# Kernel tuning notes

Measured on AMD Instinct MI355X. Metric: run time of the kernel, lower is better.

## Reference

```python
import jax, jax.numpy as jnp
import numpy as np

N_REF = 4

def setup_inputs() -> dict:
    key = jax.random.key(0)
    ks = jax.random.split(key, 6)
    B, C, H, W = 4, 256, 64, 64
    s = 1.0 / np.sqrt(C)
    return {
        'x': jax.random.normal(ks[0], (B, C, H, W), jnp.float32),
        'Wq': jax.random.normal(ks[1], (C, C), jnp.float32) * s,
        'bq': jnp.zeros((C,), jnp.float32),
        'Wk': jax.random.normal(ks[2], (C, C), jnp.float32) * s,
        'bk': jnp.zeros((C,), jnp.float32),
        'Wv': jax.random.normal(ks[3], (C, C), jnp.float32) * s,
        'bv': jnp.zeros((C,), jnp.float32),
        'Woff': jax.random.normal(ks[4], (2 * N_REF, C), jnp.float32) * s,
        'boff': jnp.zeros((2 * N_REF,), jnp.float32),
    }

def _proj(x, W, b):
    # 1x1 conv == channel-mixing linear: [B,C,H,W] -> [B,O,H,W]
    return jnp.einsum('oc,bchw->bohw', W, x) + b[None, :, None, None]

def reference(x, Wq, bq, Wk, bk, Wv, bv, Woff, boff):
    B, C, H, W = x.shape
    n = N_REF
    HW = H * W
    Q = _proj(x, Wq, bq)
    K = _proj(x, Wk, bk)
    V = _proj(x, Wv, bv)
    offsets = _proj(Q, Woff, boff).reshape(B, n, 2, H, W)
    grid_h, grid_w = jnp.meshgrid(jnp.arange(H), jnp.arange(W), indexing='ij')
    ref_x = jnp.clip(jnp.round(grid_w[None, None] + offsets[:, :, 0]).astype(jnp.int32), 0, W - 1)
    ref_y = jnp.clip(jnp.round(grid_h[None, None] + offsets[:, :, 1]).astype(jnp.int32), 0, H - 1)
    ref_idx = (ref_y * W + ref_x).reshape(B, n, HW)          # [B,n,HW]
    K_flat = K.reshape(B, C, HW)
    V_flat = V.reshape(B, C, HW)
    # gather along spatial dim -> [B,C,n,HW]
    idx = ref_idx[:, None, :, :]                              # [B,1,n,HW]
    K_g = jnp.take_along_axis(K_flat[:, :, None, :], idx, axis=3)
    V_g = jnp.take_along_axis(V_flat[:, :, None, :], idx, axis=3)
    Q_flat = Q.reshape(B, C, HW)
    attn = jnp.einsum('bch,bcnh->bnh', Q_flat, K_g)
    attn = jax.nn.softmax(attn, axis=1)
    out = jnp.einsum('bnh,bcnh->bch', attn, V_g)
    return out.reshape(B, C, H, W)
```

## Files before the change

### kernel.cpp

```cpp
#include <hip/hip_runtime.h>
#include <math.h>

#define B_DIM   4
#define C_DIM   256
#define H_DIM   64
#define W_DIM   64
#define HW_DIM  4096
#define NPIX    (B_DIM * HW_DIM)
#define NREF    4
#define NJ      10

typedef unsigned short u16;
typedef __attribute__((ext_vector_type(4))) unsigned short u16x4;
typedef __attribute__((ext_vector_type(8))) unsigned short u16x8;
typedef __attribute__((ext_vector_type(8))) short bf16x8;
typedef __attribute__((ext_vector_type(4))) float f32x4;

__device__ __forceinline__ u16 bf16_rne(float f) {
    unsigned u = __float_as_uint(f);
    u = u + 0x7FFFu + ((u >> 16) & 1u);
    return (u16)(u >> 16);
}
__device__ __forceinline__ float bf16_tof(u16 h) {
    return __uint_as_float(((unsigned)h) << 16);
}
__device__ __forceinline__ void gload16(const void* g, void* l) {
    __builtin_amdgcn_global_load_lds(
        (const __attribute__((address_space(1))) void*)g,
        (__attribute__((address_space(3))) void*)l, 16, 0, 0);
}

__global__ __launch_bounds__(256) void prep1_kernel(
    const float* __restrict__ Wq, const float* __restrict__ bq,
    const float* __restrict__ Wk, const float* __restrict__ bk,
    const float* __restrict__ Woff, const float* __restrict__ boff,
    double* __restrict__ Weffp, double* __restrict__ beff,
    double* __restrict__ Mt)
{
    const int bx = blockIdx.x;
    const int t  = threadIdx.x;

    if (bx < 4 * NJ) {
        const int j  = bx >> 2;
        const int q  = bx & 3;
        const int o0 = q * 64;
        const float* Avec = (j < 8) ? (Woff + j * C_DIM) : ((j == 8) ? bq : bk);
        const float* Bmat = (j == 8) ? Wk : Wq;
        double s0 = 0, s1 = 0, s2 = 0, s3 = 0;
        for (int o = o0; o < o0 + 64; o += 4) {
            s0 += (double)Avec[o + 0] * (double)Bmat[(size_t)(o + 0) * C_DIM + t];
            s1 += (double)Avec[o + 1] * (double)Bmat[(size_t)(o + 1) * C_DIM + t];
            s2 += (double)Avec[o + 2] * (double)Bmat[(size_t)(o + 2) * C_DIM + t];
            s3 += (double)Avec[o + 3] * (double)Bmat[(size_t)(o + 3) * C_DIM + t];
        }
        Weffp[(size_t)(q * NJ + j) * C_DIM + t] = (s0 + s1) + (s2 + s3);

        if (q == 0 && j <= 8) {
            __shared__ double red[256];
            red[t] = (j < 8) ? (double)Woff[j * C_DIM + t] * (double)bq[t]
                             : (double)bq[t] * (double)bk[t];
            __syncthreads();
            for (int st = 128; st > 0; st >>= 1) {
                if (t < st) red[t] += red[t + st];
                __syncthreads();
            }
            if (t == 0) beff[j] = (j < 8) ? red[0] + (double)boff[j] : red[0];
        }
    } else {
        const int c = bx - 4 * NJ;
        __shared__ float wqcol[256];
        wqcol[t] = Wq[(size_t)t * C_DIM + c];
        __syncthreads();
        double a0 = 0, a1 = 0, a2 = 0, a3 = 0;
        for (int o = 0; o < C_DIM; o += 4) {
            a0 += (double)wqcol[o + 0] * (double)Wk[(size_t)(o + 0) * C_DIM + t];
            a1 += (double)wqcol[o + 1] * (double)Wk[(size_t)(o + 1) * C_DIM + t];
            a2 += (double)wqcol[o + 2] * (double)Wk[(size_t)(o + 2) * C_DIM + t];
            a3 += (double)wqcol[o + 3] * (double)Wk[(size_t)(o + 3) * C_DIM + t];
        }
        Mt[(size_t)c * C_DIM + t] = (a0 + a1) + (a2 + a3);
    }
}

__global__ __launch_bounds__(256) void prep2_kernel(
    const double* __restrict__ Mt, const float* __restrict__ Wv,
    u16* __restrict__ Bswh, u16* __restrict__ Bswl)
{
    const int T     = blockIdx.x;
    const int kt    = T & 3;
    const int ntile = (T >> 2) & 1;
    const int mat   = T >> 3;
    const int n0 = ntile * 128, k0 = kt * 64;
    const int t  = threadIdx.x;
    u16* dh = Bswh + (size_t)T * 8192;
    u16* dl = Bswl + (size_t)T * 8192;

#pragma unroll
    for (int it = 0; it < 4; ++it) {
        const int s   = it * 256 + t;
        const int row = s >> 3;
        const int ch  = s & 7;
        const int kk  = k0 + (ch ^ (row & 7)) * 8;
        float v[8];
        if (mat == 0) {
            const double* src = Mt + (size_t)(n0 + row) * C_DIM + kk;
#pragma unroll
            for (int i = 0; i < 8; ++i) v[i] = (float)src[i];
        } else {
            const float* src = Wv + (size_t)(n0 + row) * C_DIM + kk;
#pragma unroll
            for (int i = 0; i < 8; ++i) v[i] = src[i];
        }
        u16x8 hv, lv;
#pragma unroll
        for (int i = 0; i < 8; ++i) {
            hv[i] = bf16_rne(v[i]);
            lv[i] = bf16_rne(v[i] - bf16_tof(hv[i]));
        }
        *(u16x8*)(dh + (size_t)s * 8) = hv;
        if (mat == 0) *(u16x8*)(dl + (size_t)s * 8) = lv;
    }
}

__global__ __launch_bounds__(256) void xsplit_kernel(
    const float* __restrict__ x, const double* __restrict__ Weffp,
    u16* __restrict__ xh, u16* __restrict__ xl, double* __restrict__ part)
{
    __shared__ float  tile[64][65];
    __shared__ double wf[NJ][64];
    const int b   = blockIdx.z;
    const int cy  = blockIdx.y;
    const int c0  = cy * 64;
    const int hw0 = blockIdx.x * 64;
    const int t   = threadIdx.x;
    const int r4  = t >> 6;
    const int col = t & 63;

#pragma unroll
    for (int i = 0; i < 16; ++i) {
        const int row = i * 4 + r4;
        tile[row][col] = x[((size_t)b * C_DIM + c0 + row) * HW_DIM + hw0 + col];
    }
    for (int d = t; d < NJ * 64; d += 256) {
        const int jj = d >> 6, cc = d & 63;
        ((double*)wf)[d] = Weffp[(size_t)(0 * NJ + jj) * C_DIM + c0 + cc]
                         + Weffp[(size_t)(1 * NJ + jj) * C_DIM + c0 + cc]
                         + Weffp[(size_t)(2 * NJ + jj) * C_DIM + c0 + cc]
                         + Weffp[(size_t)(3 * NJ + jj) * C_DIM + c0 + cc];
    }
    __syncthreads();

#pragma unroll
    for (int i = 0; i < 16; ++i) {
        const int hwr = i * 4 + r4;
        const float v = tile[col][hwr];
        const u16 h = bf16_rne(v);
        const float lo = v - bf16_tof(h);
        const size_t o = ((size_t)b * HW_DIM + hw0 + hwr) * C_DIM + c0 + col;
        xh[o] = h;
        xl[o] = bf16_rne(lo);
    }

    const int p = col, g = r4;
    double a0 = 0, a1 = 0, a2 = 0;
    for (int c = 0; c < 64; ++c) {
        const double xv = (double)tile[c][p];
        a0 += wf[2 * g][c] * xv;
        a1 += wf[2 * g + 1][c] * xv;
        if (g < 2) a2 += wf[8 + g][c] * xv;
    }
    const int pix = b * HW_DIM + hw0 + p;
    part[(size_t)(cy * NJ + 2 * g) * NPIX + pix]     = a0;
    part[(size_t)(cy * NJ + 2 * g + 1) * NPIX + pix] = a1;
    if (g < 2) part[(size_t)(cy * NJ + 8 + g) * NPIX + pix] = a2;
}

__global__ __launch_bounds__(256) void idx_kernel(
    const double* __restrict__ part, const double* __restrict__ beff,
    int* __restrict__ idx_buf, float* __restrict__ kqf, float* __restrict__ vqf)
{
    const int pix = blockIdx.x * 256 + threadIdx.x;
    const int hw  = pix & (HW_DIM - 1);
    const int h   = hw >> 6;
    const int w   = hw & 63;

    double o[8];
#pragma unroll
    for (int j = 0; j < 8; ++j)
        o[j] = part[(size_t)(0 * NJ + j) * NPIX + pix] + part[(size_t)(1 * NJ + j) * NPIX + pix]
             + part[(size_t)(2 * NJ + j) * NPIX + pix] + part[(size_t)(3 * NJ + j) * NPIX + pix]
             + beff[j];

    int r[NREF];
#pragma unroll
    for (int n = 0; n < NREF; ++n) {
        const float ox = (float)o[2 * n];
        const float oy = (float)o[2 * n + 1];
        int rx = (int)rintf((float)w + ox);
        int ry = (int)rintf((float)h + oy);
        rx = min(max(rx, 0), W_DIM - 1);
        ry = min(max(ry, 0), H_DIM - 1);
        r[n] = ry * W_DIM + rx;
    }
    int4 outv; outv.x = r[0]; outv.y = r[1]; outv.z = r[2]; outv.w = r[3];
    *(int4*)(idx_buf + (size_t)pix * 4) = outv;

    const double kq = part[(size_t)(0 * NJ + 8) * NPIX + pix] + part[(size_t)(1 * NJ + 8) * NPIX + pix]
                    + part[(size_t)(2 * NJ + 8) * NPIX + pix] + part[(size_t)(3 * NJ + 8) * NPIX + pix];
    const double vq = part[(size_t)(0 * NJ + 9) * NPIX + pix] + part[(size_t)(1 * NJ + 9) * NPIX + pix]
                    + part[(size_t)(2 * NJ + 9) * NPIX + pix] + part[(size_t)(3 * NJ + 9) * NPIX + pix]
                    + beff[8];
    kqf[pix] = (float)kq;
    vqf[pix] = (float)vq;
}

__global__ __launch_bounds__(256) void qkv_mfma(
    const u16* __restrict__ xh, const u16* __restrict__ xl,
    const u16* __restrict__ Bswh, const u16* __restrict__ Bswl,
    const float* __restrict__ bv,
    float* __restrict__ Kpt, float* __restrict__ Vt)
{
    const int mat   = blockIdx.z;
    const int ntile = blockIdx.y;
    const int m0    = blockIdx.x * 64;
    const int n0    = ntile * 128;
    const bool three = (mat == 0);
    float* Out = mat ? Vt : Kpt;

    __shared__ u16 lds[24576];
    u16* Ah = lds;
    u16* Al = lds + 4096;
    u16* Bh = lds + 8192;
    u16* Bl = lds + 16384;

    const int t    = threadIdx.x;
    const int lane = t & 63;
    const int wv   = t >> 6;
    const int wm   = (wv >> 1) * 32;
    const int wn   = (wv & 1) * 64;

    f32x4 acc[2][4] = {};

    for (int kt = 0; kt < 4; ++kt) {
        const int k0 = kt * 64;
        const size_t Tb = (size_t)((mat * 2 + ntile) * 4 + kt) * 8192;

#pragma unroll
        for (int it = 0; it < 2; ++it) {
            const int s   = it * 256 + t;
            const int row = s >> 3;
            const int sch = (s & 7) ^ (row & 7);
            const size_t goff = (size_t)(m0 + row) * C_DIM + k0 + sch * 8;
            gload16(xh + goff, (char*)Ah + s * 16);
            if (three) gload16(xl + goff, (char*)Al + s * 16);
        }
#pragma unroll
        for (int it = 0; it < 4; ++it) {
            const int s = it * 256 + t;
            gload16(Bswh + Tb + (size_t)s * 8, (char*)Bh + s * 16);
            if (three) gload16(Bswl + Tb + (size_t)s * 8, (char*)Bl + s * 16);
        }
        __syncthreads();

#pragma unroll
        for (int ks = 0; ks < 2; ++ks) {
            bf16x8 afh[2], afl[2], bfh[4], bfl[4];
#pragma unroll
            for (int mt = 0; mt < 2; ++mt) {
                const int row = wm + mt * 16 + (lane & 15);
                const int ch  = (ks * 4 + (lane >> 4)) ^ (row & 7);
                const int off = row * 128 + ch * 16;
                afh[mt] = *(const bf16x8*)((const char*)Ah + off);
                if (three) afl[mt] = *(const bf16x8*)((const char*)Al + off);
            }
#pragma unroll
            for (int nt = 0; nt < 4; ++nt) {
                const int row = wn + nt * 16 + (lane & 15);
                const int ch  = (ks * 4 + (lane >> 4)) ^ (row & 7);
                const int off = row * 128 + ch * 16;
                bfh[nt] = *(const bf16x8*)((const char*)Bh + off);
                if (three) bfl[nt] = *(const bf16x8*)((const char*)Bl + off);
            }
#pragma unroll
            for (int mt = 0; mt < 2; ++mt)
#pragma unroll
                for (int nt = 0; nt < 4; ++nt) {
                    acc[mt][nt] = __builtin_amdgcn_mfma_f32_16x16x32_bf16(afh[mt], bfh[nt], acc[mt][nt], 0, 0, 0);
                    if (three) {
                        acc[mt][nt] = __builtin_amdgcn_mfma_f32_16x16x32_bf16(afh[mt], bfl[nt], acc[mt][nt], 0, 0, 0);
                        acc[mt][nt] = __builtin_amdgcn_mfma_f32_16x16x32_bf16(afl[mt], bfh[nt], acc[mt][nt], 0, 0, 0);
                    }
                }
        }
        __syncthreads();
    }

    const int col = lane & 15;
    const int rg  = (lane >> 4) * 4;
#pragma unroll
    for (int nt = 0; nt < 4; ++nt) {
        const int n = n0 + wn + nt * 16 + col;
        const float bias = mat ? bv[n] : 0.0f;
#pragma unroll
        for (int mt = 0; mt < 2; ++mt) {
            const int m = m0 + wm + mt * 16 + rg;
#pragma unroll
            for (int r = 0; r < 4; ++r)
                Out[(size_t)(m + r) * C_DIM + n] = acc[mt][nt][r] + bias;
        }
    }
}

__global__ __launch_bounds__(1024) void attn_kernel(
    const u16*   __restrict__ xh,
    const u16*   __restrict__ xl,
    const float* __restrict__ Kpt,
    const float* __restrict__ Vt,
    const int*   __restrict__ idx_buf,
    const float* __restrict__ kqf,
    const float* __restrict__ vqf,
    float* __restrict__ out)
{
    __shared__ float trans[16][260];

    const int t    = threadIdx.x;
    const int wave = t >> 6;
    const int lane = t & 63;

    const int pix0 = blockIdx.x * 16;
    const int b    = pix0 / HW_DIM;
    const int hw   = (pix0 % HW_DIM) + wave;
    const int pix  = b * HW_DIM + hw;

    const u16x4 hv = *(const u16x4*)(xh + (size_t)pix * C_DIM + lane * 4);
    const u16x4 lv = *(const u16x4*)(xl + (size_t)pix * C_DIM + lane * 4);
    float q[4];
#pragma unroll
    for (int i = 0; i < 4; ++i) q[i] = bf16_tof(hv[i]) + bf16_tof(lv[i]);

    const int4 iv = *(const int4*)(idx_buf + (size_t)pix * 4);
    int idx[NREF] = {iv.x, iv.y, iv.z, iv.w};
    const float vq = vqf[pix];

    float logit[NREF];
#pragma unroll
    for (int n = 0; n < NREF; ++n) {
        const float* krow = Kpt + ((size_t)b * HW_DIM + idx[n]) * C_DIM;
        float4 kv = *(const float4*)(krow + lane * 4);
        float lp = fmaf(q[3], kv.w, fmaf(q[2], kv.z, fmaf(q[1], kv.y, q[0] * kv.x)));
#pragma unroll
        for (int off = 1; off < 64; off <<= 1) lp += __shfl_xor(lp, off);
        logit[n] = lp + kqf[(size_t)b * HW_DIM + idx[n]] + vq;
    }

    float mx = fmaxf(fmaxf(logit[0], logit[1]), fmaxf(logit[2], logit[3]));
    float e[NREF], s = 0.0f;
#pragma unroll
    for (int n = 0; n < NREF; ++n) { e[n] = expf(logit[n] - mx); s += e[n]; }
    float wgt[NREF];
#pragma unroll
    for (int n = 0; n < NREF; ++n) wgt[n] = e[n] / s;

    float o4[4] = {0.f, 0.f, 0.f, 0.f};
#pragma unroll
    for (int n = 0; n < NREF; ++n) {
        const float* vrow = Vt + ((size_t)b * HW_DIM + idx[n]) * C_DIM;
        float4 vv = *(const float4*)(vrow + lane * 4);
        o4[0] = fmaf(wgt[n], vv.x, o4[0]);
        o4[1] = fmaf(wgt[n], vv.y, o4[1]);
        o4[2] = fmaf(wgt[n], vv.z, o4[2]);
        o4[3] = fmaf(wgt[n], vv.w, o4[3]);
    }

    *(float4*)&trans[wave][lane * 4] = *(float4*)o4;
    __syncthreads();

    float* ob = out + (size_t)b * C_DIM * HW_DIM + (pix0 % HW_DIM);
    const int px = t & 15;
#pragma unroll
    for (int cc = 0; cc < C_DIM; cc += 64) {
        const int c = cc + (t >> 4);
        ob[(size_t)c * HW_DIM + px] = trans[px][c];
    }
}

extern "C" void kernel_launch(void* const* d_in, const int* in_sizes, int n_in,
                              void* d_out, int out_size, void* d_ws, size_t ws_size,
                              hipStream_t stream) {
    const float* x    = (const float*)d_in[0];
    const float* Wq   = (const float*)d_in[1];
    const float* bq   = (const float*)d_in[2];
    const float* Wk   = (const float*)d_in[3];
    const float* bk   = (const float*)d_in[4];
    const float* Wv   = (const float*)d_in[5];
    const float* bv   = (const float*)d_in[6];
    const float* Woff = (const float*)d_in[7];
    const float* boff = (const float*)d_in[8];
    float* out = (float*)d_out;

    char* ws = (char*)d_ws;
    float*  Kpt   = (float*)ws;
    float*  Vt    = (float*)(ws + (size_t)16 * 1024 * 1024);
    u16*    xh    = (u16*)  (ws + (size_t)48 * 1024 * 1024);
    u16*    xl    = (u16*)  (ws + (size_t)56 * 1024 * 1024);
    char*   aux   = ws + (size_t)64 * 1024 * 1024;
    double* Weffp = (double*)(aux);
    double* beff  = (double*)(aux + 128 * 1024);
    int*    idxb  = (int*)   (aux + 192 * 1024);
    float*  kqf   = (float*) (aux + 448 * 1024);
    float*  vqf   = (float*) (aux + 512 * 1024);
    u16*    Bswh  = (u16*)   (aux + 576 * 1024);
    u16*    Bswl  = (u16*)   (aux + 832 * 1024);
    double* Mt    = (double*)(aux + 1088 * 1024);
    double* part  = (double*)(aux + 2 * 1024 * 1024);

    prep1_kernel<<<dim3(4 * NJ + 256), dim3(256), 0, stream>>>(
        Wq, bq, Wk, bk, Woff, boff, Weffp, beff, Mt);
    prep2_kernel<<<dim3(16), dim3(256), 0, stream>>>(Mt, Wv, Bswh, Bswl);
    xsplit_kernel<<<dim3(HW_DIM / 64, C_DIM / 64, B_DIM), dim3(256), 0, stream>>>(
        x, Weffp, xh, xl, part);
    idx_kernel<<<dim3(NPIX / 256), dim3(256), 0, stream>>>(part, beff, idxb, kqf, vqf);
    qkv_mfma<<<dim3(NPIX / 64, 2, 2), dim3(256), 0, stream>>>(
        xh, xl, Bswh, Bswl, bv, Kpt, Vt);
    attn_kernel<<<dim3(NPIX / 16), dim3(1024), 0, stream>>>(
        xh, xl, Kpt, Vt, idxb, kqf, vqf, out);
}
```

Measured before the change: 69.71 us.

## Merge prep kernels, widen QKV GEMM tile to full N, store V in bf16

The two weight-prep kernels become one launch. Wq^T·Wk is now computed directly in fp32 with an LDS-tiled GEMM and written out in swizzled hi/lo bf16 form, which removes the double-precision Mt intermediate. The QKV MFMA kernel now covers all 256 output columns per block, so the A tile is loaded once instead of twice, at the cost of more LDS and accumulators per block. V is stored as bf16 to halve gather traffic in the attention kernel, which loses some precision in V. The M matrix is now accumulated in fp32 rather than fp64.

```diff
diff --git a/kernel.cpp b/kernel.cpp
--- a/kernel.cpp
+++ b/kernel.cpp
@@ -30,12 +30,13 @@
         (__attribute__((address_space(3))) void*)l, 16, 0, 0);
 }
 
-__global__ __launch_bounds__(256) void prep1_kernel(
+__global__ __launch_bounds__(256) void prep_kernel(
     const float* __restrict__ Wq, const float* __restrict__ bq,
     const float* __restrict__ Wk, const float* __restrict__ bk,
+    const float* __restrict__ Wv,
     const float* __restrict__ Woff, const float* __restrict__ boff,
     double* __restrict__ Weffp, double* __restrict__ beff,
-    double* __restrict__ Mt)
+    u16* __restrict__ Bswh, u16* __restrict__ Bswl)
 {
     const int bx = blockIdx.x;
     const int t  = threadIdx.x;
@@ -66,59 +67,92 @@
             }
             if (t == 0) beff[j] = (j < 8) ? red[0] + (double)boff[j] : red[0];
         }
+    } else if (bx < 72) {
+        __shared__ float wq_s[64][32];
+        __shared__ float wk_s[64][64];
+        const int sub   = bx - 40;
+        const int T     = sub >> 2;
+        const int nsub  = sub & 3;
+        const int ntile = T >> 2;
+        const int kt    = T & 3;
+        const int nb    = ntile * 128 + nsub * 32;
+        const int kb    = kt * 64;
+
+        const int tx = t & 15;
+        const int ty = t >> 4;
+
+        float acc[2][4] = {};
+
+        for (int oc = 0; oc < 4; ++oc) {
+            const int o0 = oc * 64;
+#pragma unroll
+            for (int i = 0; i < 2; ++i) {
+                const int s = i * 256 + t;
+                const int row = s >> 3, c4 = (s & 7) * 4;
+                *(float4*)&wq_s[row][c4] =
+                    *(const float4*)(Wq + (size_t)(o0 + row) * C_DIM + nb + c4);
+            }
+#pragma unroll
+            for (int i = 0; i < 4; ++i) {
+                const int s = i * 256 + t;
+                const int row = s >> 4, c4 = (s & 15) * 4;
+                *(float4*)&wk_s[row][c4] =
+                    *(const float4*)(Wk + (size_t)(o0 + row) * C_DIM + kb + c4);
+            }
+            __syncthreads();
+#pragma unroll 4
+            for (int oo = 0; oo < 64; ++oo) {
+                const float2 a = *(const float2*)&wq_s[oo][ty * 2];
+                const float4 b4 = *(const float4*)&wk_s[oo][tx * 4];
+                acc[0][0] = fmaf(a.x, b4.x, acc[0][0]);
+                acc[0][1] = fmaf(a.x, b4.y, acc[0][1]);
+                acc[0][2] = fmaf(a.x, b4.z, acc[0][2]);
+                acc[0][3] = fmaf(a.x, b4.w, acc[0][3]);
+                acc[1][0] = fmaf(a.y, b4.x, acc[1][0]);
+                acc[1][1] = fmaf(a.y, b4.y, acc[1][1]);
+                acc[1][2] = fmaf(a.y, b4.z, acc[1][2]);
+                acc[1][3] = fmaf(a.y, b4.w, acc[1][3]);
+            }
+            __syncthreads();
+        }
+
+        u16* dh = Bswh + (size_t)T * 8192;
+        u16* dl = Bswl + (size_t)T * 8192;
+#pragma unroll
+        for (int j = 0; j < 2; ++j) {
+            const int rimg = nsub * 32 + ty * 2 + j;
+            const int base = rimg * 64 + (((tx >> 1) ^ (rimg & 7)) * 8) + (tx & 1) * 4;
+            u16x4 hv, lv;
+#pragma unroll
+            for (int i = 0; i < 4; ++i) {
+                hv[i] = bf16_rne(acc[j][i]);
+                lv[i] = bf16_rne(acc[j][i] - bf16_tof(hv[i]));
+            }
+            *(u16x4*)(dh + base) = hv;
+            *(u16x4*)(dl + base) = lv;
+        }
     } else {
-        const int c = bx - 4 * NJ;
-        __shared__ float wqcol[256];
-        wqcol[t] = Wq[(size_t)t * C_DIM + c];
-        __syncthreads();
-        double a0 = 0, a1 = 0, a2 = 0, a3 = 0;
-        for (int o = 0; o < C_DIM; o += 4) {
-            a0 += (double)wqcol[o + 0] * (double)Wk[(size_t)(o + 0) * C_DIM + t];
-            a1 += (double)wqcol[o + 1] * (double)Wk[(size_t)(o + 1) * C_DIM + t];
-            a2 += (double)wqcol[o + 2] * (double)Wk[(size_t)(o + 2) * C_DIM + t];
-            a3 += (double)wqcol[o + 3] * (double)Wk[(size_t)(o + 3) * C_DIM + t];
-        }
-        Mt[(size_t)c * C_DIM + t] = (a0 + a1) + (a2 + a3);
-    }
-}
-
-__global__ __launch_bounds__(256) void prep2_kernel(
-    const double* __restrict__ Mt, const float* __restrict__ Wv,
-    u16* __restrict__ Bswh, u16* __restrict__ Bswl)
-{
-    const int T     = blockIdx.x;
-    const int kt    = T & 3;
-    const int ntile = (T >> 2) & 1;
-    const int mat   = T >> 3;
-    const int n0 = ntile * 128, k0 = kt * 64;
-    const int t  = threadIdx.x;
-    u16* dh = Bswh + (size_t)T * 8192;
-    u16* dl = Bswl + (size_t)T * 8192;
-
-#pragma unroll
-    for (int it = 0; it < 4; ++it) {
-        const int s   = it * 256 + t;
-        const int row = s >> 3;
-        const int ch  = s & 7;
-        const int kk  = k0 + (ch ^ (row & 7)) * 8;
-        float v[8];
-        if (mat == 0) {
-            const double* src = Mt + (size_t)(n0 + row) * C_DIM + kk;
-#pragma unroll
-            for (int i = 0; i < 8; ++i) v[i] = (float)src[i];
-        } else {
-            const float* src = Wv + (size_t)(n0 + row) * C_DIM + kk;
-#pragma unroll
-            for (int i = 0; i < 8; ++i) v[i] = src[i];
-        }
-        u16x8 hv, lv;
-#pragma unroll
-        for (int i = 0; i < 8; ++i) {
-            hv[i] = bf16_rne(v[i]);
-            lv[i] = bf16_rne(v[i] - bf16_tof(hv[i]));
-        }
-        *(u16x8*)(dh + (size_t)s * 8) = hv;
-        if (mat == 0) *(u16x8*)(dl + (size_t)s * 8) = lv;
+        const int ti    = bx - 72;
+        const int kt    = ti & 3;
+        const int ntile = (ti >> 2) & 1;
+        const int Timg  = 8 + ti;
+        const int n0 = ntile * 128, k0 = kt * 64;
+        u16* dh = Bswh + (size_t)Timg * 8192;
+#pragma unroll
+        for (int it = 0; it < 4; ++it) {
+            const int s   = it * 256 + t;
+            const int row = s >> 3;
+            const int ch  = s & 7;
+            const int kk  = k0 + (ch ^ (row & 7)) * 8;
+            const float4 w0 = *(const float4*)(Wv + (size_t)(n0 + row) * C_DIM + kk);
+            const float4 w1 = *(const float4*)(Wv + (size_t)(n0 + row) * C_DIM + kk + 4);
+            u16x8 hv;
+            hv[0] = bf16_rne(w0.x); hv[1] = bf16_rne(w0.y);
+            hv[2] = bf16_rne(w0.z); hv[3] = bf16_rne(w0.w);
+            hv[4] = bf16_rne(w1.x); hv[5] = bf16_rne(w1.y);
+            hv[6] = bf16_rne(w1.z); hv[7] = bf16_rne(w1.w);
+            *(u16x8*)(dh + (size_t)s * 8) = hv;
+        }
     }
 }
 
@@ -218,32 +252,28 @@
     const u16* __restrict__ xh, const u16* __restrict__ xl,
     const u16* __restrict__ Bswh, const u16* __restrict__ Bswl,
     const float* __restrict__ bv,
-    float* __restrict__ Kpt, float* __restrict__ Vt)
+    float* __restrict__ Kpt, u16* __restrict__ Vtb)
 {
-    const int mat   = blockIdx.z;
-    const int ntile = blockIdx.y;
-    const int m0    = blockIdx.x * 64;
-    const int n0    = ntile * 128;
+    const int mat = blockIdx.x & 1;
+    const int m0  = (blockIdx.x >> 1) * 64;
     const bool three = (mat == 0);
-    float* Out = mat ? Vt : Kpt;
-
-    __shared__ u16 lds[24576];
+
+    __shared__ u16 lds[40960];
     u16* Ah = lds;
     u16* Al = lds + 4096;
     u16* Bh = lds + 8192;
-    u16* Bl = lds + 16384;
+    u16* Bl = lds + 24576;
 
     const int t    = threadIdx.x;
     const int lane = t & 63;
     const int wv   = t >> 6;
     const int wm   = (wv >> 1) * 32;
-    const int wn   = (wv & 1) * 64;
-
-    f32x4 acc[2][4] = {};
+    const int wn   = (wv & 1) * 128;
+
+    f32x4 acc[2][8] = {};
 
     for (int kt = 0; kt < 4; ++kt) {
         const int k0 = kt * 64;
-        const size_t Tb = (size_t)((mat * 2 + ntile) * 4 + kt) * 8192;
 
 #pragma unroll
         for (int it = 0; it < 2; ++it) {
@@ -255,16 +285,19 @@
             if (three) gload16(xl + goff, (char*)Al + s * 16);
         }
 #pragma unroll
-        for (int it = 0; it < 4; ++it) {
-            const int s = it * 256 + t;
-            gload16(Bswh + Tb + (size_t)s * 8, (char*)Bh + s * 16);
-            if (three) gload16(Bswl + Tb + (size_t)s * 8, (char*)Bl + s * 16);
+        for (int it = 0; it < 8; ++it) {
+            const int s  = it * 256 + t;
+            const int ni = s >> 10;
+            const int sl = s & 1023;
+            const size_t Tb = (size_t)((mat * 2 + ni) * 4 + kt) * 8192;
+            gload16(Bswh + Tb + (size_t)sl * 8, (char*)Bh + s * 16);
+            if (three) gload16(Bswl + Tb + (size_t)sl * 8, (char*)Bl + s * 16);
         }
         __syncthreads();
 
 #pragma unroll
         for (int ks = 0; ks < 2; ++ks) {
-            bf16x8 afh[2], afl[2], bfh[4], bfl[4];
+            bf16x8 afh[2], afl[2];
 #pragma unroll
             for (int mt = 0; mt < 2; ++mt) {
                 const int row = wm + mt * 16 + (lane & 15);
@@ -274,23 +307,29 @@
                 if (three) afl[mt] = *(const bf16x8*)((const char*)Al + off);
             }
 #pragma unroll
-            for (int nt = 0; nt < 4; ++nt) {
-                const int row = wn + nt * 16 + (lane & 15);
-                const int ch  = (ks * 4 + (lane >> 4)) ^ (row & 7);
-                const int off = row * 128 + ch * 16;
-                bfh[nt] = *(const bf16x8*)((const char*)Bh + off);
-                if (three) bfl[nt] = *(const bf16x8*)((const char*)Bl + off);
-            }
-#pragma unroll
-            for (int mt = 0; mt < 2; ++mt)
+            for (int ng = 0; ng < 2; ++ng) {
+                bf16x8 bfh[4], bfl[4];
 #pragma unroll
                 for (int nt = 0; nt < 4; ++nt) {
-                    acc[mt][nt] = __builtin_amdgcn_mfma_f32_16x16x32_bf16(afh[mt], bfh[nt], acc[mt][nt], 0, 0, 0);
-                    if (three) {
-                        acc[mt][nt] = __builtin_amdgcn_mfma_f32_16x16x32_bf16(afh[mt], bfl[nt], acc[mt][nt], 0, 0, 0);
-                        acc[mt][nt] = __builtin_amdgcn_mfma_f32_16x16x32_bf16(afl[mt], bfh[nt], acc[mt][nt], 0, 0, 0);
+                    const int row = wn + ng * 64 + nt * 16 + (lane & 15);
+                    const int ch  = (ks * 4 + (lane >> 4)) ^ (row & 7);
+                    const int off = row * 128 + ch * 16;
+                    bfh[nt] = *(const bf16x8*)((const char*)Bh + off);
+                    if (three) bfl[nt] = *(const bf16x8*)((const char*)Bl + off);
+                }
+#pragma unroll
+                for (int mt = 0; mt < 2; ++mt)
+#pragma unroll
+                    for (int nt = 0; nt < 4; ++nt) {
+                        f32x4 a = acc[mt][ng * 4 + nt];
+                        a = __builtin_amdgcn_mfma_f32_16x16x32_bf16(afh[mt], bfh[nt], a, 0, 0, 0);
+                        if (three) {
+                            a = __builtin_amdgcn_mfma_f32_16x16x32_bf16(afh[mt], bfl[nt], a, 0, 0, 0);
+                            a = __builtin_amdgcn_mfma_f32_16x16x32_bf16(afl[mt], bfh[nt], a, 0, 0, 0);
+                        }
+                        acc[mt][ng * 4 + nt] = a;
                     }
-                }
+            }
         }
         __syncthreads();
     }
@@ -298,24 +337,29 @@
     const int col = lane & 15;
     const int rg  = (lane >> 4) * 4;
 #pragma unroll
-    for (int nt = 0; nt < 4; ++nt) {
-        const int n = n0 + wn + nt * 16 + col;
-        const float bias = mat ? bv[n] : 0.0f;
-#pragma unroll
-        for (int mt = 0; mt < 2; ++mt) {
-            const int m = m0 + wm + mt * 16 + rg;
-#pragma unroll
-            for (int r = 0; r < 4; ++r)
-                Out[(size_t)(m + r) * C_DIM + n] = acc[mt][nt][r] + bias;
-        }
-    }
+    for (int ng = 0; ng < 2; ++ng)
+#pragma unroll
+        for (int nt = 0; nt < 4; ++nt) {
+            const int n = wn + ng * 64 + nt * 16 + col;
+            const float bias = mat ? bv[n] : 0.0f;
+#pragma unroll
+            for (int mt = 0; mt < 2; ++mt) {
+                const int m = m0 + wm + mt * 16 + rg;
+#pragma unroll
+                for (int r = 0; r < 4; ++r) {
+                    const float v = acc[mt][ng * 4 + nt][r] + bias;
+                    if (mat) Vtb[(size_t)(m + r) * C_DIM + n] = bf16_rne(v);
+                    else     Kpt[(size_t)(m + r) * C_DIM + n] = v;
+                }
+            }
+        }
 }
 
 __global__ __launch_bounds__(1024) void attn_kernel(
     const u16*   __restrict__ xh,
     const u16*   __restrict__ xl,
     const float* __restrict__ Kpt,
-    const float* __restrict__ Vt,
+    const u16*   __restrict__ Vtb,
     const int*   __restrict__ idx_buf,
     const float* __restrict__ kqf,
     const float* __restrict__ vqf,
@@ -364,12 +408,11 @@
     float o4[4] = {0.f, 0.f, 0.f, 0.f};
 #pragma unroll
     for (int n = 0; n < NREF; ++n) {
-        const float* vrow = Vt + ((size_t)b * HW_DIM + idx[n]) * C_DIM;
-        float4 vv = *(const float4*)(vrow + lane * 4);
-        o4[0] = fmaf(wgt[n], vv.x, o4[0]);
-        o4[1] = fmaf(wgt[n], vv.y, o4[1]);
-        o4[2] = fmaf(wgt[n], vv.z, o4[2]);
-        o4[3] = fmaf(wgt[n], vv.w, o4[3]);
+        const u16x4 vv = *(const u16x4*)(Vtb + ((size_t)b * HW_DIM + idx[n]) * C_DIM + lane * 4);
+        o4[0] = fmaf(wgt[n], bf16_tof(vv[0]), o4[0]);
+        o4[1] = fmaf(wgt[n], bf16_tof(vv[1]), o4[1]);
+        o4[2] = fmaf(wgt[n], bf16_tof(vv[2]), o4[2]);
+        o4[3] = fmaf(wgt[n], bf16_tof(vv[3]), o4[3]);
     }
 
     *(float4*)&trans[wave][lane * 4] = *(float4*)o4;
@@ -400,7 +443,7 @@
 
     char* ws = (char*)d_ws;
     float*  Kpt   = (float*)ws;
-    float*  Vt    = (float*)(ws + (size_t)16 * 1024 * 1024);
+    u16*    Vtb   = (u16*)  (ws + (size_t)16 * 1024 * 1024);
     u16*    xh    = (u16*)  (ws + (size_t)48 * 1024 * 1024);
     u16*    xl    = (u16*)  (ws + (size_t)56 * 1024 * 1024);
     char*   aux   = ws + (size_t)64 * 1024 * 1024;
@@ -411,17 +454,15 @@
     float*  vqf   = (float*) (aux + 512 * 1024);
     u16*    Bswh  = (u16*)   (aux + 576 * 1024);
     u16*    Bswl  = (u16*)   (aux + 832 * 1024);
-    double* Mt    = (double*)(aux + 1088 * 1024);
     double* part  = (double*)(aux + 2 * 1024 * 1024);
 
-    prep1_kernel<<<dim3(4 * NJ + 256), dim3(256), 0, stream>>>(
-        Wq, bq, Wk, bk, Woff, boff, Weffp, beff, Mt);
-    prep2_kernel<<<dim3(16), dim3(256), 0, stream>>>(Mt, Wv, Bswh, Bswl);
+    prep_kernel<<<dim3(80), dim3(256), 0, stream>>>(
+        Wq, bq, Wk, bk, Wv, Woff, boff, Weffp, beff, Bswh, Bswl);
     xsplit_kernel<<<dim3(HW_DIM / 64, C_DIM / 64, B_DIM), dim3(256), 0, stream>>>(
         x, Weffp, xh, xl, part);
     idx_kernel<<<dim3(NPIX / 256), dim3(256), 0, stream>>>(part, beff, idxb, kqf, vqf);
-    qkv_mfma<<<dim3(NPIX / 64, 2, 2), dim3(256), 0, stream>>>(
-        xh, xl, Bswh, Bswl, bv, Kpt, Vt);
+    qkv_mfma<<<dim3((NPIX / 64) * 2), dim3(256), 0, stream>>>(
+        xh, xl, Bswh, Bswl, bv, Kpt, Vtb);
     attn_kernel<<<dim3(NPIX / 16), dim3(1024), 0, stream>>>(
-        xh, xl, Kpt, Vt, idxb, kqf, vqf, out);
-}
+        xh, xl, Kpt, Vtb, idxb, kqf, vqf, out);
+}
```

Measured after the change: 64.67 us (median of 5 runs). 7.2% less time.
